# Performance work log

Measured on AMD Instinct MI355X. Metric: run time of the kernel, lower is better.

## Reference

```python
import jax, jax.numpy as jnp
import numpy as np

B, S = 32, 1024
D_MODEL, N_LABEL, D_H, D_HH, N_HEAD, N_LAYER = 1024, 8192, 64, 64, 16, 4
EPS = 1e-12

def _sq(x):
    return jnp.sum(x * x, axis=-1, keepdims=True)

def expmap0(v):
    # exponential map at the origin of the Poincare ball (c=1)
    n = jnp.sqrt(jnp.clip(_sq(v), EPS))
    return jnp.tanh(n) * v / n

def p2k(p):
    # Poincare -> Klein
    return 2.0 * p / (1.0 + _sq(p))

def k2p(k):
    # Klein -> Poincare
    return k / (1.0 + jnp.sqrt(jnp.clip(1.0 - _sq(k), EPS)))

def hyperboloid(x, klein=False):
    # lift Poincare (default) or Klein point to the hyperboloid (Lorentz) model
    sq = _sq(x)
    if klein:
        d = jnp.sqrt(jnp.clip(1.0 - sq, EPS))
        return jnp.concatenate([jnp.ones_like(sq), x], -1) / d
    return jnp.concatenate([1.0 + sq, 2.0 * x], -1) / jnp.clip(1.0 - sq, EPS)

def dist_h(u, v):
    # pairwise Lorentzian distance: u [..., n, D+1], v [..., m, D+1] -> [..., n, m]
    inner = jnp.matmul(u, jnp.swapaxes(v, -1, -2)) \
        - 2.0 * u[..., 0][..., :, None] * v[..., 0][..., None, :]
    return jnp.arccosh(jnp.clip(-inner, 1.0 + 1e-6))

def setup_inputs():
    key = jax.random.key(0)
    ks = jax.random.split(key, 12)
    def lin(k, i, o):
        return jax.random.normal(k, (i, o), jnp.float32) / float(np.sqrt(i))
    return {
        "e": jax.random.normal(ks[0], (B, S, D_MODEL), jnp.float32),
        # label embeddings kept strictly inside the unit ball (pretrained-style)
        "label": (jax.random.uniform(ks[1], (N_LABEL, D_H), jnp.float32) * 2.0 - 1.0) * float(0.5 / np.sqrt(D_H)),
        "tc_w1": lin(ks[2], D_MODEL, 2 * D_MODEL), "tc_b1": jnp.zeros((2 * D_MODEL,), jnp.float32),
        "tc_w2": lin(ks[3], 2 * D_MODEL, D_HH * N_HEAD), "tc_b2": jnp.zeros((D_HH * N_HEAD,), jnp.float32),
        "hyp_w": lin(ks[4], D_HH, D_H), "hyp_b": jnp.zeros((D_H,), jnp.float32),
        "agg_w1": lin(ks[5], N_HEAD, 2 * N_HEAD), "agg_b1": jnp.zeros((2 * N_HEAD,), jnp.float32),
        "agg_w2": lin(ks[6], 2 * N_HEAD, 2 * N_HEAD), "agg_b2": jnp.zeros((2 * N_HEAD,), jnp.float32),
        "agg_w3": lin(ks[7], 2 * N_HEAD, N_HEAD), "agg_b3": jnp.zeros((N_HEAD,), jnp.float32),
        "agg_w4": lin(ks[8], N_HEAD, 1), "agg_b4": jnp.zeros((1,), jnp.float32),
        "y": jax.random.randint(ks[9], (B, 1), 0, N_LABEL, jnp.int32),
        "mask_text": jax.random.randint(ks[10], (B, S), 0, 2, jnp.int32),
        "mask_label": jax.random.randint(ks[11], (B, N_LABEL), 0, 2, jnp.int32),
    }

def reference(e, label, tc_w1, tc_b1, tc_w2, tc_b2, hyp_w, hyp_b,
              agg_w1, agg_b1, agg_w2, agg_b2, agg_w3, agg_b3, agg_w4, agg_b4,
              y, mask_text, mask_label):
    # textconv + torch-style .view(B, n_head, S, d_hh) (pure reshape)
    h = jax.nn.relu(e @ tc_w1 + tc_b1) @ tc_w2 + tc_b2            # [B,S,H*d_hh]
    h = h.reshape(B, N_HEAD, S, D_HH)
    ek = expmap0(h @ hyp_w + hyp_b)                                # [B,H,S,d_h] Poincare ball
    q = jnp.broadcast_to(label[y][:, None], (B, N_HEAD, 1, D_H))   # [B,H,1,d_h]
    mask = mask_text[:, None, None, :] > 0                         # [B,1,1,S]
    kh = hyperboloid(ek)                                           # [B,H,S,d_h+1]
    vk = p2k(ek)                                                   # Klein coords for midpoint
    gamma = 1.0 / jnp.sqrt(jnp.clip(1.0 - _sq(vk), EPS))           # Lorentz factors [B,H,S,1]
    g = gamma[..., 0][:, :, None, :]                               # [B,H,1,S]
    # HyperbolicPathSearch: n_layer steps of distance-softmax + Einstein midpoint
    for _ in range(N_LAYER):
        scores = -dist_h(hyperboloid(q), kh)                       # [B,H,1,S]
        w = jax.nn.softmax(jnp.where(mask, scores, -1e9), axis=-1)
        wg = w * g
        mid = jnp.einsum('bhqs,bhsd->bhqd', wg, vk) / jnp.sum(wg, -1, keepdims=True)
        q = k2p(mid)
    # distance from attention output to every label embedding
    d = dist_h(hyperboloid(q), hyperboloid(label)[None, None])     # [B,H,1,n_label]
    d = jnp.squeeze(d, 2).transpose(0, 2, 1)                       # [B,n_label,H]
    x = jax.nn.relu(d @ agg_w1 + agg_b1)
    x = jax.nn.relu(x @ agg_w2 + agg_b2)
    x = jax.nn.relu(x @ agg_w3 + agg_b3)
    out = (x @ agg_w4 + agg_b4)[..., 0]                            # [B,n_label]
    return jnp.where(mask_label > 0, out, -500.0)
```

## Files before the change

### kernel.cpp

```cpp
#include <hip/hip_runtime.h>
#include <stdint.h>


typedef unsigned short u16;
typedef unsigned char u8;
typedef __attribute__((ext_vector_type(4))) float f32x4;
typedef __attribute__((ext_vector_type(4))) int i32x4;
typedef __attribute__((ext_vector_type(8))) int i32x8;

#define DEVI static __device__ __forceinline__

DEVI float bf2f(u16 u) { return __uint_as_float(((unsigned int)u) << 16); }
DEVI u16 f2bfbits(float f) {
  unsigned int x = __float_as_uint(f);
  unsigned int r = x + 0x7fffu + ((x >> 16) & 1u);
  return (u16)(r >> 16);
}
DEVI u8 f2fp8(float f) {
  return (u8)(__builtin_amdgcn_cvt_pk_fp8_f32(f, 0.f, 0, false) & 0xff);
}
DEVI unsigned int pack4_fp8(float a, float b, float c, float d) {
  int r = __builtin_amdgcn_cvt_pk_fp8_f32(a, b, 0, false);
  r = __builtin_amdgcn_cvt_pk_fp8_f32(c, d, r, true);
  return (unsigned int)r;
}

typedef __attribute__((address_space(1))) unsigned int gu32;
typedef __attribute__((address_space(3))) unsigned int su32;
DEVI void lds_cp16(const void* g, void* l) {
  __builtin_amdgcn_global_load_lds((gu32*)g, (su32*)l, 16, 0, 0);
}

__global__ __launch_bounds__(256) void prep_kernel(
    const float* __restrict__ e, const float* __restrict__ w1,
    const float* __restrict__ w2, const float* __restrict__ b2,
    const float* __restrict__ hw, const float* __restrict__ hb,
    const float* __restrict__ label,
    u8* __restrict__ e8, u8* __restrict__ w1T8, u8* __restrict__ w2eT8,
    float* __restrict__ beff, u16* __restrict__ lh) {
  __shared__ float t[64][65];
  const int blk = blockIdx.x;
  const int tid = threadIdx.x;

  if (blk >= 673) {
    int gi = (blk - 673) * 256 + tid;
    const float4* in = (const float4*)e + (size_t)gi * 4;
    float4 f0 = in[0], f1 = in[1], f2 = in[2], f3 = in[3];
    uint4 o;
    o.x = pack4_fp8(f0.x, f0.y, f0.z, f0.w);
    o.y = pack4_fp8(f1.x, f1.y, f1.z, f1.w);
    o.z = pack4_fp8(f2.x, f2.y, f2.z, f2.w);
    o.w = pack4_fp8(f3.x, f3.y, f3.z, f3.w);
    ((uint4*)e8)[gi] = o;
  } else if (blk < 512) {
    int c0 = (blk & 31) * 64, r0 = (blk >> 5) * 64;
    int tx = tid & 63, ty = tid >> 6;
#pragma unroll
    for (int i = 0; i < 16; i++) {
      int r = i * 4 + ty;
      t[r][tx] = w1[(size_t)(r0 + r) * 2048 + c0 + tx];
    }
    __syncthreads();
#pragma unroll
    for (int i = 0; i < 16; i++) {
      int c = i * 4 + ty;
      w1T8[(size_t)(c0 + c) * 1024 + r0 + tx] = f2fp8(t[tx][c] * 32.f);
    }
  } else if (blk < 640) {
    int bw = blk - 512;
    int ch = bw >> 3, kb = bw & 7;
    int k = kb * 256 + tid;
    float row[64];
    const float4* rp = (const float4*)(w2 + (size_t)k * 1024 + ch * 64);
#pragma unroll
    for (int i = 0; i < 16; i++) {
      float4 f = rp[i];
      row[i * 4] = f.x; row[i * 4 + 1] = f.y; row[i * 4 + 2] = f.z; row[i * 4 + 3] = f.w;
    }
    for (int o = 0; o < 64; o++) {
      float a = 0.f;
#pragma unroll
      for (int d = 0; d < 64; d++) a = fmaf(row[d], hw[d * 64 + o], a);
      w2eT8[(size_t)(ch * 64 + o) * 2048 + k] = f2fp8(a * 64.f);
    }
  } else if (blk == 640) {
    for (int n = tid; n < 1024; n += 256) {
      int ch = n >> 6, o = n & 63;
      float a = hb[o];
#pragma unroll
      for (int d = 0; d < 64; d++) a += b2[ch * 64 + d] * hw[d * 64 + o];
      beff[n] = a;
    }
  } else {
    int l = (blk - 641) * 256 + tid;
    const float4* lp = (const float4*)(label + (size_t)l * 64);
    float v[64]; float sq = 0.f;
#pragma unroll
    for (int i = 0; i < 16; i++) {
      float4 f = lp[i];
      v[i * 4] = f.x; v[i * 4 + 1] = f.y; v[i * 4 + 2] = f.z; v[i * 4 + 3] = f.w;
      sq += f.x * f.x + f.y * f.y + f.z * f.z + f.w * f.w;
    }
    float dd = fmaxf(1.f - sq, 1e-12f);
    lh[l] = f2bfbits((1.f + sq) / dd);
#pragma unroll
    for (int c = 0; c < 64; c++) lh[(size_t)(c + 1) * 8192 + l] = f2bfbits(2.f * v[c] / dd);
  }
}

template <int MODE>
__global__ __launch_bounds__(256, 4) void gemm_mx(
    const u8* __restrict__ A, const u8* __restrict__ Bt,
    const float* __restrict__ bias, u8* __restrict__ C,
    u16* __restrict__ kh, int N, int K, unsigned int sb_scale) {
  __shared__ __attribute__((aligned(16))) u8 SM[32768];
  u8* As = SM;
  u8* Bs = SM + 16384;
  const int tid = threadIdx.x;
  const int wave = tid >> 6, lane = tid & 63;
  const int fr = lane & 15, q = lane >> 4;
  const int nblk = N >> 7;
  const int g = blockIdx.x;
  const int xcd = g & 7;
  const int t = g >> 3;
  const int per = (gridDim.x >> 3) / nblk;
  const int bm = xcd * per + t / nblk;
  const int bn = t % nblk;
  const size_t m0 = (size_t)bm * 128;
  const int n0 = bn * 128;
  const int wm = (wave >> 1) << 6, wn = (wave & 1) << 6;
  f32x4 acc[4][4] = {};

  const int srow = tid >> 3;
  const int schunk = (tid & 7) ^ (srow & 7);
  const u8* Ap = A + (m0 + srow) * (size_t)K + schunk * 16;
  const u8* Bp = Bt + ((size_t)n0 + srow) * K + schunk * 16;

  const int aL = (wm + fr) * 128 + ((((q << 1)) ^ (fr & 7)) << 4);
  const int bL = (wn + fr) * 128 + ((((q << 1)) ^ (fr & 7)) << 4);

  for (int kk = 0; kk < K; kk += 128) {
#pragma unroll
    for (int c = 0; c < 4; c++) {
      lds_cp16(Ap + (size_t)c * 32 * K, As + c * 4096 + wave * 1024);
      lds_cp16(Bp + (size_t)c * 32 * K, Bs + c * 4096 + wave * 1024);
    }
    Ap += 128; Bp += 128;
    __syncthreads();
    i32x8 af[4], bf[4];
#pragma unroll
    for (int t2 = 0; t2 < 4; t2++) {
      i32x4 lo = *(const i32x4*)(As + aL + t2 * 2048);
      i32x4 hi = *(const i32x4*)(As + (aL ^ 16) + t2 * 2048);
      af[t2] = __builtin_shufflevector(lo, hi, 0, 1, 2, 3, 4, 5, 6, 7);
      i32x4 lo2 = *(const i32x4*)(Bs + bL + t2 * 2048);
      i32x4 hi2 = *(const i32x4*)(Bs + (bL ^ 16) + t2 * 2048);
      bf[t2] = __builtin_shufflevector(lo2, hi2, 0, 1, 2, 3, 4, 5, 6, 7);
    }
#pragma unroll
    for (int i = 0; i < 4; i++)
#pragma unroll
      for (int j = 0; j < 4; j++)
        acc[i][j] = __builtin_amdgcn_mfma_scale_f32_16x16x128_f8f6f4(
            af[i], bf[j], acc[i][j], 0, 0,
            0, 0x7F7F7F7F,
            0, (int)sb_scale);
    __syncthreads();
  }

  if constexpr (MODE == 0) {
#pragma unroll
    for (int j = 0; j < 4; j++) {
      int col = n0 + wn + j * 16 + fr;
      float bv = bias[col];
#pragma unroll
      for (int i = 0; i < 4; i++) {
#pragma unroll
        for (int r = 0; r < 4; r++) {
          size_t row = m0 + wm + i * 16 + q * 4 + r;
          C[row * N + col] = f2fp8(fmaxf(acc[i][j][r] + bv, 0.f));
        }
      }
    }
  } else {
    u16* ew = (u16*)SM;
    u16* k0w = (u16*)(SM + 9216);
    const int head = (n0 + wn) >> 6;
    const int rb = (int)m0 + wm;
    const int b = rb >> 10, s0 = rb & 1023;
    u16* base = kh + (size_t)(b * 16 + head) * 65 * 1024;
    float bv[4];
#pragma unroll
    for (int j = 0; j < 4; j++) bv[j] = bias[n0 + wn + j * 16 + fr];

    float ff[4][4];
#pragma unroll
    for (int i = 0; i < 4; i++) {
#pragma unroll
      for (int r = 0; r < 4; r++) {
        float v0 = acc[i][0][r] + bv[0];
        float v1 = acc[i][1][r] + bv[1];
        float v2 = acc[i][2][r] + bv[2];
        float v3 = acc[i][3][r] + bv[3];
        float ss = v0 * v0 + v1 * v1 + v2 * v2 + v3 * v3;
        ss += __shfl_xor(ss, 1); ss += __shfl_xor(ss, 2);
        ss += __shfl_xor(ss, 4); ss += __shfl_xor(ss, 8);
        float n = sqrtf(fmaxf(ss, 1e-12f));
        float ex = __expf(-2.f * n);
        float th = (1.f - ex) / (1.f + ex);
        float sq = th * th;
        float dd = fmaxf(1.f - sq, 1e-12f);
        ff[i][r] = 2.f * (th / n) / dd;
        if (fr == 0) k0w[wave * 64 + i * 16 + q * 4 + r] = f2bfbits((1.f + sq) / dd);
      }
    }
#pragma unroll
    for (int j = 0; j < 4; j++) {
#pragma unroll
      for (int i = 0; i < 4; i++)
#pragma unroll
        for (int r = 0; r < 4; r++) {
          int trow = i * 16 + q * 4 + r;
          ew[wave * 1056 + fr * 66 + trow] =
              f2bfbits((acc[i][j][r] + bv[j]) * ff[i][r]);
        }
      __syncthreads();
#pragma unroll
      for (int it = 0; it < 8; it++) {
        int c2 = it * 2 + (lane >> 5);
        int tok = (lane & 31) * 2;
        unsigned int dat = *(const unsigned int*)(ew + wave * 1056 + c2 * 66 + tok);
        *(unsigned int*)(base + (size_t)(1 + j * 16 + c2) * 1024 + s0 + tok) = dat;
      }
      __syncthreads();
    }
    if (lane < 32) {
      unsigned int dat = *(const unsigned int*)(k0w + wave * 64 + lane * 2);
      *(unsigned int*)(base + s0 + lane * 2) = dat;
    }
  }
}

__global__ __launch_bounds__(256, 2) void attn_kernel(
    const u16* __restrict__ kh, const float* __restrict__ label,
    const int* __restrict__ y, const int* __restrict__ mask_text,
    float* __restrict__ qh_out) {
  const int g = blockIdx.x;
  const int b = (g & 7) * 4 + ((g >> 3) & 3);
  const int h = g >> 5;
  const int bh = b * 16 + h;
  const int tid = threadIdx.x, lane = tid & 63, wave = tid >> 6;
  __shared__ float qh[65], rtmp[4], redp[4][65];
  const u16* khb = kh + (size_t)bh * 65 * 1024;

  float kh0[4];
  unsigned int khp[4][32];
  int mt[4];
#pragma unroll
  for (int r = 0; r < 4; r++) {
    int s = r * 256 + tid;
    mt[r] = mask_text[b * 1024 + s];
    kh0[r] = bf2f(khb[s]);
#pragma unroll
    for (int k = 0; k < 32; k++) {
      unsigned int lo = khb[(1 + 2 * k) * 1024 + s];
      unsigned int hi = khb[(2 + 2 * k) * 1024 + s];
      khp[r][k] = lo | (hi << 16);
    }
  }

  if (wave == 0) {
    float qv = label[(size_t)y[b] * 64 + lane];
    float sq = qv * qv;
#pragma unroll
    for (int d = 1; d < 64; d <<= 1) sq += __shfl_xor(sq, d);
    float dd = fmaxf(1.f - sq, 1e-12f);
    qh[lane + 1] = 2.f * qv / dd;
    if (lane == 0) qh[0] = (1.f + sq) / dd;
  }
  __syncthreads();

  for (int layer = 0; layer < 4; layer++) {
    float q0 = qh[0];
    float inn[4];
#pragma unroll
    for (int r = 0; r < 4; r++) inn[r] = -q0 * kh0[r];
#pragma unroll
    for (int k = 0; k < 32; k++) {
      float qa = qh[1 + 2 * k], qb = qh[2 + 2 * k];
#pragma unroll
      for (int r = 0; r < 4; r++) {
        unsigned int p = khp[r][k];
        inn[r] = fmaf(qa, __uint_as_float(p << 16),
                 fmaf(qb, __uint_as_float(p & 0xffff0000u), inn[r]));
      }
    }
    float w[4]; float lmax = -3e38f;
#pragma unroll
    for (int r = 0; r < 4; r++) {
      float x = fmaxf(-inn[r], 1.f + 1e-6f);
      float sco = -acoshf(x);
      sco = (mt[r] > 0) ? sco : -1e9f;
      w[r] = sco;
      lmax = fmaxf(lmax, sco);
    }
#pragma unroll
    for (int d = 1; d < 64; d <<= 1) lmax = fmaxf(lmax, __shfl_xor(lmax, d));
    if (lane == 0) rtmp[wave] = lmax;
    __syncthreads();
    float m = fmaxf(fmaxf(rtmp[0], rtmp[1]), fmaxf(rtmp[2], rtmp[3]));
#pragma unroll
    for (int r = 0; r < 4; r++) w[r] = __expf(w[r] - m);

    float p0 = w[0] * kh0[0] + w[1] * kh0[1] + w[2] * kh0[2] + w[3] * kh0[3];
#pragma unroll
    for (int d = 1; d < 64; d <<= 1) p0 += __shfl_xor(p0, d);
    if (lane == 0) redp[wave][0] = p0;
#pragma unroll
    for (int k = 0; k < 32; k++) {
      float pa = 0.f, pb = 0.f;
#pragma unroll
      for (int r = 0; r < 4; r++) {
        unsigned int p = khp[r][k];
        pa = fmaf(w[r], __uint_as_float(p << 16), pa);
        pb = fmaf(w[r], __uint_as_float(p & 0xffff0000u), pb);
      }
#pragma unroll
      for (int d = 1; d < 64; d <<= 1) pa += __shfl_xor(pa, d);
#pragma unroll
      for (int d = 1; d < 64; d <<= 1) pb += __shfl_xor(pb, d);
      if (lane == 0) { redp[wave][1 + 2 * k] = pa; redp[wave][2 + 2 * k] = pb; }
    }
    __syncthreads();

    if (wave == 0) {
      float denom = redp[0][0] + redp[1][0] + redp[2][0] + redp[3][0];
      float num = redp[0][lane + 1] + redp[1][lane + 1] + redp[2][lane + 1] + redp[3][lane + 1];
      float mid = num / denom;
      float kl = mid * mid;
#pragma unroll
      for (int d = 1; d < 64; d <<= 1) kl += __shfl_xor(kl, d);
      float u = sqrtf(fmaxf(1.f - kl, 1e-12f));
      float pc = mid / (1.f + u);
      float sp = kl / ((1.f + u) * (1.f + u));
      float dd = fmaxf(1.f - sp, 1e-12f);
      qh[lane + 1] = 2.f * pc / dd;
      if (lane == 0) qh[0] = (1.f + sp) / dd;
    }
    __syncthreads();
  }
  if (tid < 65) qh_out[(size_t)bh * 65 + tid] = qh[tid];
}

__global__ __launch_bounds__(256) void label_mlp(
    const float* __restrict__ qh, const u16* __restrict__ lh,
    const float* __restrict__ w1, const float* __restrict__ b1,
    const float* __restrict__ w2, const float* __restrict__ b2,
    const float* __restrict__ w3, const float* __restrict__ b3,
    const float* __restrict__ w4, const float* __restrict__ b4,
    const int* __restrict__ mask_label, float* __restrict__ out) {
  int blk = blockIdx.x;
  int b = blk >> 5, lb = blk & 31;
  int l = lb * 256 + threadIdx.x;
  const float* qb = qh + (size_t)b * 1040;

  float inner[16];
  float l0 = bf2f(lh[l]);
#pragma unroll
  for (int h = 0; h < 16; h++) inner[h] = -qb[h * 65] * l0;
  for (int c = 1; c < 65; c++) {
    float lc = bf2f(lh[(size_t)c * 8192 + l]);
#pragma unroll
    for (int h = 0; h < 16; h++) inner[h] = fmaf(qb[h * 65 + c], lc, inner[h]);
  }
  float d[16];
#pragma unroll
  for (int h = 0; h < 16; h++) d[h] = acoshf(fmaxf(-inner[h], 1.f + 1e-6f));

  float x1[32];
#pragma unroll
  for (int o = 0; o < 32; o++) {
    float a = b1[o];
#pragma unroll
    for (int h = 0; h < 16; h++) a = fmaf(d[h], w1[h * 32 + o], a);
    x1[o] = fmaxf(a, 0.f);
  }
  float x2[32];
#pragma unroll
  for (int o = 0; o < 32; o++) {
    float a = b2[o];
#pragma unroll
    for (int i = 0; i < 32; i++) a = fmaf(x1[i], w2[i * 32 + o], a);
    x2[o] = fmaxf(a, 0.f);
  }
  float x3[16];
#pragma unroll
  for (int o = 0; o < 16; o++) {
    float a = b3[o];
#pragma unroll
    for (int i = 0; i < 32; i++) a = fmaf(x2[i], w3[i * 16 + o], a);
    x3[o] = fmaxf(a, 0.f);
  }
  float acc = b4[0];
#pragma unroll
  for (int h = 0; h < 16; h++) acc = fmaf(x3[h], w4[h], acc);
  out[(size_t)b * 8192 + l] = (mask_label[(size_t)b * 8192 + l] > 0) ? acc : -500.0f;
}

extern "C" void kernel_launch(void* const* d_in, const int* in_sizes, int n_in,
                              void* d_out, int out_size, void* d_ws, size_t ws_size,
                              hipStream_t stream) {
  const float* e     = (const float*)d_in[0];
  const float* label = (const float*)d_in[1];
  const float* tc_w1 = (const float*)d_in[2];
  const float* tc_b1 = (const float*)d_in[3];
  const float* tc_w2 = (const float*)d_in[4];
  const float* tc_b2 = (const float*)d_in[5];
  const float* hyp_w = (const float*)d_in[6];
  const float* hyp_b = (const float*)d_in[7];
  const float* aw1 = (const float*)d_in[8];
  const float* ab1 = (const float*)d_in[9];
  const float* aw2 = (const float*)d_in[10];
  const float* ab2 = (const float*)d_in[11];
  const float* aw3 = (const float*)d_in[12];
  const float* ab3 = (const float*)d_in[13];
  const float* aw4 = (const float*)d_in[14];
  const float* ab4 = (const float*)d_in[15];
  const int* y          = (const int*)d_in[16];
  const int* mask_text  = (const int*)d_in[17];
  const int* mask_label = (const int*)d_in[18];
  float* out = (float*)d_out;

  char* ws = (char*)d_ws;
  u8*    X8    = (u8*)(ws + 0);
  float* qh    = (float*)(ws + 0);
  u16*   kh    = (u16*)(ws + 67108864ull);
  u8*    e8    = (u8*)(ws + 135266304ull);
  u8*    w1T8  = (u8*)(ws + 168820736ull);
  u8*    w2eT8 = (u8*)(ws + 170917888ull);
  float* beff  = (float*)(ws + 173015040ull);
  u16*   lh    = (u16*)(ws + 173019136ull);

  prep_kernel<<<673 + 8192, 256, 0, stream>>>(e, tc_w1, tc_w2, tc_b2, hyp_w, hyp_b,
                                              label, e8, w1T8, w2eT8, beff, lh);
  gemm_mx<0><<<4096, 256, 0, stream>>>(e8, w1T8, tc_b1, X8, nullptr, 2048, 1024,
                                       0x7A7A7A7Au);
  gemm_mx<1><<<2048, 256, 0, stream>>>(X8, w2eT8, beff, nullptr, kh, 1024, 2048,
                                       0x79797979u);
  attn_kernel<<<512, 256, 0, stream>>>(kh, label, y, mask_text, qh);
  label_mlp<<<1024, 256, 0, stream>>>(qh, lh, aw1, ab1, aw2, ab2, aw3, ab3, aw4, ab4,
                                      mask_label, out);
}
```

Measured before the change: 544.4 us.

## Interleave hyperboloid key and label channels in 8-wide groups for 16-byte loads

Changes the layout of the hyperboloid keys (kh) and label lifts (lh) from one plane per channel to groups of 8 bf16 channels packed per token. Channel 0 moves to its own array. The GEMM epilogue, prep kernel, attention kernel and label MLP now write and read these with uint4 accesses instead of 2-byte or 4-byte scalar accesses. This cuts the number of memory transactions on the attention key load and the label-distance pass. The cost is repacking logic in the epilogues and a new workspace layout whose offsets must not overlap.

```diff
diff --git a/kernel.cpp b/kernel.cpp
--- a/kernel.cpp
+++ b/kernel.cpp
@@ -37,7 +37,7 @@
     const float* __restrict__ hw, const float* __restrict__ hb,
     const float* __restrict__ label,
     u8* __restrict__ e8, u8* __restrict__ w1T8, u8* __restrict__ w2eT8,
-    float* __restrict__ beff, u16* __restrict__ lh) {
+    float* __restrict__ beff, u16* __restrict__ lh0, u16* __restrict__ lhg) {
   __shared__ float t[64][65];
   const int blk = blockIdx.x;
   const int tid = threadIdx.x;
@@ -102,9 +102,16 @@
       sq += f.x * f.x + f.y * f.y + f.z * f.z + f.w * f.w;
     }
     float dd = fmaxf(1.f - sq, 1e-12f);
-    lh[l] = f2bfbits((1.f + sq) / dd);
-#pragma unroll
-    for (int c = 0; c < 64; c++) lh[(size_t)(c + 1) * 8192 + l] = f2bfbits(2.f * v[c] / dd);
+    lh0[l] = f2bfbits((1.f + sq) / dd);
+    float sc = 2.f / dd;
+#pragma unroll
+    for (int g = 0; g < 8; g++) {
+      unsigned int o0 = f2bfbits(v[8 * g + 0] * sc) | ((unsigned int)f2bfbits(v[8 * g + 1] * sc) << 16);
+      unsigned int o1 = f2bfbits(v[8 * g + 2] * sc) | ((unsigned int)f2bfbits(v[8 * g + 3] * sc) << 16);
+      unsigned int o2 = f2bfbits(v[8 * g + 4] * sc) | ((unsigned int)f2bfbits(v[8 * g + 5] * sc) << 16);
+      unsigned int o3 = f2bfbits(v[8 * g + 6] * sc) | ((unsigned int)f2bfbits(v[8 * g + 7] * sc) << 16);
+      ((uint4*)lhg)[(size_t)g * 8192 + l] = make_uint4(o0, o1, o2, o3);
+    }
   }
 }
 
@@ -112,7 +119,8 @@
 __global__ __launch_bounds__(256, 4) void gemm_mx(
     const u8* __restrict__ A, const u8* __restrict__ Bt,
     const float* __restrict__ bias, u8* __restrict__ C,
-    u16* __restrict__ kh, int N, int K, unsigned int sb_scale) {
+    u16* __restrict__ khg, u16* __restrict__ kh0,
+    int N, int K, unsigned int sb_scale) {
   __shared__ __attribute__((aligned(16))) u8 SM[32768];
   u8* As = SM;
   u8* Bs = SM + 16384;
@@ -188,7 +196,7 @@
     const int head = (n0 + wn) >> 6;
     const int rb = (int)m0 + wm;
     const int b = rb >> 10, s0 = rb & 1023;
-    u16* base = kh + (size_t)(b * 16 + head) * 65 * 1024;
+    u16* gbase = khg + (size_t)(b * 16 + head) * 65536;
     float bv[4];
 #pragma unroll
     for (int j = 0; j < 4; j++) bv[j] = bias[n0 + wn + j * 16 + fr];
@@ -226,23 +234,27 @@
         }
       __syncthreads();
 #pragma unroll
-      for (int it = 0; it < 8; it++) {
-        int c2 = it * 2 + (lane >> 5);
-        int tok = (lane & 31) * 2;
-        unsigned int dat = *(const unsigned int*)(ew + wave * 1056 + c2 * 66 + tok);
-        *(unsigned int*)(base + (size_t)(1 + j * 16 + c2) * 1024 + s0 + tok) = dat;
+      for (int it = 0; it < 2; it++) {
+        const u16* eb = ew + wave * 1056 + it * 8 * 66 + lane;
+        unsigned int o0 = eb[0]   | ((unsigned int)eb[66]  << 16);
+        unsigned int o1 = eb[132] | ((unsigned int)eb[198] << 16);
+        unsigned int o2 = eb[264] | ((unsigned int)eb[330] << 16);
+        unsigned int o3 = eb[396] | ((unsigned int)eb[462] << 16);
+        *(uint4*)(gbase + ((size_t)(j * 2 + it) * 1024 + s0 + lane) * 8) =
+            make_uint4(o0, o1, o2, o3);
       }
       __syncthreads();
     }
     if (lane < 32) {
       unsigned int dat = *(const unsigned int*)(k0w + wave * 64 + lane * 2);
-      *(unsigned int*)(base + s0 + lane * 2) = dat;
+      *(unsigned int*)(kh0 + (size_t)(b * 16 + head) * 1024 + s0 + lane * 2) = dat;
     }
   }
 }
 
 __global__ __launch_bounds__(256, 2) void attn_kernel(
-    const u16* __restrict__ kh, const float* __restrict__ label,
+    const u16* __restrict__ khg, const u16* __restrict__ kh0,
+    const float* __restrict__ label,
     const int* __restrict__ y, const int* __restrict__ mask_text,
     float* __restrict__ qh_out) {
   const int g = blockIdx.x;
@@ -251,21 +263,24 @@
   const int bh = b * 16 + h;
   const int tid = threadIdx.x, lane = tid & 63, wave = tid >> 6;
   __shared__ float qh[65], rtmp[4], redp[4][65];
-  const u16* khb = kh + (size_t)bh * 65 * 1024;
-
-  float kh0[4];
+  const u16* khb = khg + (size_t)bh * 65536;
+  const u16* k0b = kh0 + (size_t)bh * 1024;
+
+  float kh0r[4];
   unsigned int khp[4][32];
   int mt[4];
 #pragma unroll
   for (int r = 0; r < 4; r++) {
     int s = r * 256 + tid;
     mt[r] = mask_text[b * 1024 + s];
-    kh0[r] = bf2f(khb[s]);
-#pragma unroll
-    for (int k = 0; k < 32; k++) {
-      unsigned int lo = khb[(1 + 2 * k) * 1024 + s];
-      unsigned int hi = khb[(2 + 2 * k) * 1024 + s];
-      khp[r][k] = lo | (hi << 16);
+    kh0r[r] = bf2f(k0b[s]);
+#pragma unroll
+    for (int gg = 0; gg < 8; gg++) {
+      uint4 v = *(const uint4*)(khb + ((size_t)gg * 1024 + s) * 8);
+      khp[r][gg * 4 + 0] = v.x;
+      khp[r][gg * 4 + 1] = v.y;
+      khp[r][gg * 4 + 2] = v.z;
+      khp[r][gg * 4 + 3] = v.w;
     }
   }
 
@@ -284,7 +299,7 @@
     float q0 = qh[0];
     float inn[4];
 #pragma unroll
-    for (int r = 0; r < 4; r++) inn[r] = -q0 * kh0[r];
+    for (int r = 0; r < 4; r++) inn[r] = -q0 * kh0r[r];
 #pragma unroll
     for (int k = 0; k < 32; k++) {
       float qa = qh[1 + 2 * k], qb = qh[2 + 2 * k];
@@ -312,7 +327,7 @@
 #pragma unroll
     for (int r = 0; r < 4; r++) w[r] = __expf(w[r] - m);
 
-    float p0 = w[0] * kh0[0] + w[1] * kh0[1] + w[2] * kh0[2] + w[3] * kh0[3];
+    float p0 = w[0] * kh0r[0] + w[1] * kh0r[1] + w[2] * kh0r[2] + w[3] * kh0r[3];
 #pragma unroll
     for (int d = 1; d < 64; d <<= 1) p0 += __shfl_xor(p0, d);
     if (lane == 0) redp[wave][0] = p0;
@@ -353,7 +368,8 @@
 }
 
 __global__ __launch_bounds__(256) void label_mlp(
-    const float* __restrict__ qh, const u16* __restrict__ lh,
+    const float* __restrict__ qh, const u16* __restrict__ lh0,
+    const u16* __restrict__ lhg,
     const float* __restrict__ w1, const float* __restrict__ b1,
     const float* __restrict__ w2, const float* __restrict__ b2,
     const float* __restrict__ w3, const float* __restrict__ b3,
@@ -365,13 +381,23 @@
   const float* qb = qh + (size_t)b * 1040;
 
   float inner[16];
-  float l0 = bf2f(lh[l]);
+  float l0 = bf2f(lh0[l]);
 #pragma unroll
   for (int h = 0; h < 16; h++) inner[h] = -qb[h * 65] * l0;
-  for (int c = 1; c < 65; c++) {
-    float lc = bf2f(lh[(size_t)c * 8192 + l]);
-#pragma unroll
-    for (int h = 0; h < 16; h++) inner[h] = fmaf(qb[h * 65 + c], lc, inner[h]);
+#pragma unroll
+  for (int g = 0; g < 8; g++) {
+    uint4 v = *(const uint4*)(lhg + ((size_t)g * 8192 + l) * 8);
+    unsigned int pw[4] = {v.x, v.y, v.z, v.w};
+#pragma unroll
+    for (int p = 0; p < 4; p++) {
+      int k = g * 4 + p;
+      float la = __uint_as_float(pw[p] << 16);
+      float lb2 = __uint_as_float(pw[p] & 0xffff0000u);
+#pragma unroll
+      for (int h = 0; h < 16; h++)
+        inner[h] = fmaf(qb[h * 65 + 1 + 2 * k], la,
+                   fmaf(qb[h * 65 + 2 + 2 * k], lb2, inner[h]));
+    }
   }
   float d[16];
 #pragma unroll
@@ -434,20 +460,22 @@
   char* ws = (char*)d_ws;
   u8*    X8    = (u8*)(ws + 0);
   float* qh    = (float*)(ws + 0);
-  u16*   kh    = (u16*)(ws + 67108864ull);
+  u16*   khg   = (u16*)(ws + 67108864ull);
+  u16*   kh0   = (u16*)(ws + 134217728ull);
   u8*    e8    = (u8*)(ws + 135266304ull);
   u8*    w1T8  = (u8*)(ws + 168820736ull);
   u8*    w2eT8 = (u8*)(ws + 170917888ull);
   float* beff  = (float*)(ws + 173015040ull);
-  u16*   lh    = (u16*)(ws + 173019136ull);
+  u16*   lhg   = (u16*)(ws + 173019136ull);
+  u16*   lh0   = (u16*)(ws + 174067712ull);
 
   prep_kernel<<<673 + 8192, 256, 0, stream>>>(e, tc_w1, tc_w2, tc_b2, hyp_w, hyp_b,
-                                              label, e8, w1T8, w2eT8, beff, lh);
-  gemm_mx<0><<<4096, 256, 0, stream>>>(e8, w1T8, tc_b1, X8, nullptr, 2048, 1024,
-                                       0x7A7A7A7Au);
-  gemm_mx<1><<<2048, 256, 0, stream>>>(X8, w2eT8, beff, nullptr, kh, 1024, 2048,
-                                       0x79797979u);
-  attn_kernel<<<512, 256, 0, stream>>>(kh, label, y, mask_text, qh);
-  label_mlp<<<1024, 256, 0, stream>>>(qh, lh, aw1, ab1, aw2, ab2, aw3, ab3, aw4, ab4,
-                                      mask_label, out);
-}
+                                              label, e8, w1T8, w2eT8, beff, lh0, lhg);
+  gemm_mx<0><<<4096, 256, 0, stream>>>(e8, w1T8, tc_b1, X8, nullptr, nullptr,
+                                       2048, 1024, 0x7A7A7A7Au);
+  gemm_mx<1><<<2048, 256, 0, stream>>>(X8, w2eT8, beff, nullptr, khg, kh0,
+                                       1024, 2048, 0x79797979u);
+  attn_kernel<<<512, 256, 0, stream>>>(khg, kh0, label, y, mask_text, qh);
+  label_mlp<<<1024, 256, 0, stream>>>(qh, lh0, lhg, aw1, ab1, aw2, ab2, aw3, ab3,
+                                      aw4, ab4, mask_label, out);
+}
```

New measurement: 553.3 us. No clear change (+1.6%).
